# Kernel optimization log

Hardware: AMD Instinct MI355X
Metric: run time of the kernel (lower is better)

The kernel has to match this reference:

```python
import jax, jax.numpy as jnp
import numpy as np


def setup_inputs() -> dict:
    key = jax.random.key(0)
    ks = jax.random.split(key, 4)
    B, S, D, H, E = 4, 2048, 1024, 4096, 4
    sd = 1.0 / np.sqrt(D)
    sh = 1.0 / np.sqrt(H)
    return {
        "x": jax.random.normal(ks[0], (B, S, D), jnp.float32),
        "Wr": jax.random.normal(ks[1], (D, E), jnp.float32) * sd,
        "W1": jax.random.normal(ks[2], (E, D, H), jnp.float32) * sd,
        "b1": jnp.zeros((E, H), jnp.float32),
        "W2": jax.random.normal(ks[3], (E, H, D), jnp.float32) * sh,
        "b2": jnp.zeros((E, D), jnp.float32),
        "top_k": 2,
    }


def reference(x, Wr, W1, b1, W2, b2, top_k):
    # Router: softmax over experts, then top-k + renormalize (as in torch code)
    logits = jnp.einsum("bsd,de->bse", x, Wr)              # [B,S,E]
    probs = jax.nn.softmax(logits, axis=-1)
    wk, idx = jax.lax.top_k(probs, top_k)                  # [B,S,K]
    wk = wk / jnp.sum(wk, axis=-1, keepdims=True)
    # Scatter top-k weights back to dense per-expert weights [B,S,E]
    E = probs.shape[-1]
    onehot = jax.nn.one_hot(idx, E, dtype=x.dtype)         # [B,S,K,E]
    weights = jnp.einsum("bsk,bske->bse", wk, onehot)      # [B,S,E]
    # Expert MLPs (Linear-ReLU-Linear), computed dense over experts and
    # combined with the (mostly-zero) routing weights — same math as the
    # gather/scatter loop in the torch module.
    h = jax.nn.relu(jnp.einsum("bsd,edh->bseh", x, W1) + b1)   # [B,S,E,H]
    y = jnp.einsum("bseh,ehd->bsed", h, W2) + b2               # [B,S,E,D]
    out = jnp.einsum("bse,bsed->bsd", weights, y)              # [B,S,D]
    aux_loss = jnp.asarray(0.0, dtype=x.dtype)
    return out, aux_loss
```

## Files before the change

kernel.cpp:

```cpp
#include <hip/hip_runtime.h>
#include <cstdint>
#include <cstddef>

typedef _Float16 f16;
typedef __attribute__((ext_vector_type(8))) f16 f16x8;
typedef __attribute__((ext_vector_type(4))) f16 f16x4;
typedef __attribute__((ext_vector_type(4))) float f32x4;

#define M_TOK 8192
#define DDIM 1024
#define HDIM 4096
#define NEXP 4
#define TOTPAD 16896

__device__ __forceinline__ void async_copy16(const void* g, void* s) {
    __builtin_amdgcn_global_load_lds((__attribute__((address_space(1))) void*)g,
                                     (__attribute__((address_space(3))) void*)s,
                                     16, 0, 0);
}

__global__ __launch_bounds__(256) void router_kernel(
    const float* __restrict__ x, const float* __restrict__ Wr,
    float* __restrict__ wts, int* __restrict__ top2, float2* __restrict__ wpair) {
    __shared__ float wr_s[DDIM * NEXP];
    for (int i = threadIdx.x; i < DDIM * NEXP; i += 256) wr_s[i] = Wr[i];
    __syncthreads();
    const int wave = threadIdx.x >> 6, lane = threadIdx.x & 63;
    const int t = blockIdx.x * 4 + wave;
    float a0 = 0.f, a1 = 0.f, a2 = 0.f, a3 = 0.f;
    const float* xr = x + (size_t)t * DDIM;
    for (int i = 0; i < DDIM; i += 256) {
        const int d = i + lane * 4;
        const float4 v = *(const float4*)(xr + d);
        const float* w0 = &wr_s[d * 4];
        a0 += v.x * w0[0] + v.y * w0[4] + v.z * w0[8]  + v.w * w0[12];
        a1 += v.x * w0[1] + v.y * w0[5] + v.z * w0[9]  + v.w * w0[13];
        a2 += v.x * w0[2] + v.y * w0[6] + v.z * w0[10] + v.w * w0[14];
        a3 += v.x * w0[3] + v.y * w0[7] + v.z * w0[11] + v.w * w0[15];
    }
    for (int off = 32; off > 0; off >>= 1) {
        a0 += __shfl_xor(a0, off, 64);
        a1 += __shfl_xor(a1, off, 64);
        a2 += __shfl_xor(a2, off, 64);
        a3 += __shfl_xor(a3, off, 64);
    }
    if (lane == 0) {
        float lg[4] = {a0, a1, a2, a3};
        int i1 = 0;
        for (int e = 1; e < 4; ++e) if (lg[e] > lg[i1]) i1 = e;
        int i2 = -1;
        for (int e = 0; e < 4; ++e) {
            if (e == i1) continue;
            if (i2 < 0 || lg[e] > lg[i2]) i2 = e;
        }
        const float w1 = 1.0f / (1.0f + expf(lg[i2] - lg[i1]));
        float w[4] = {0.f, 0.f, 0.f, 0.f};
        w[i1] = w1; w[i2] = 1.0f - w1;
        float* o = wts + (size_t)t * 4;
        o[0] = w[0]; o[1] = w[1]; o[2] = w[2]; o[3] = w[3];
        top2[t] = i1 | (i2 << 8);
        wpair[t] = make_float2(w1, 1.0f - w1);
    }
}

__global__ __launch_bounds__(256) void count_kernel(
    const int* __restrict__ top2, int* __restrict__ meta) {
    __shared__ int lc[4];
    if (threadIdx.x < 4) lc[threadIdx.x] = 0;
    __syncthreads();
    const int t = blockIdx.x * 256 + threadIdx.x;
    const int p = top2[t];
    atomicAdd(&lc[p & 0xff], 1);
    atomicAdd(&lc[(p >> 8) & 0xff], 1);
    __syncthreads();
    if (threadIdx.x < 4) atomicAdd(&meta[threadIdx.x], lc[threadIdx.x]);
}

__global__ void offsets_kernel(int* __restrict__ meta) {
    if (threadIdx.x == 0) {
        int off = 0;
        for (int e = 0; e < 4; ++e) {
            const int c = meta[e];
            const int cp = (c + 127) & ~127;
            meta[4 + e] = cp;
            meta[8 + e] = off;
            off += cp;
        }
    }
}

__global__ __launch_bounds__(256) void fill_kernel(
    const int* __restrict__ top2, int* __restrict__ meta,
    int* __restrict__ toklist, int2* __restrict__ slotmap) {
    __shared__ int lc[4], base[4];
    if (threadIdx.x < 4) lc[threadIdx.x] = 0;
    __syncthreads();
    const int t = blockIdx.x * 256 + threadIdx.x;
    const int p = top2[t];
    const int e1 = p & 0xff, e2 = (p >> 8) & 0xff;
    const int r1 = atomicAdd(&lc[e1], 1);
    const int r2 = atomicAdd(&lc[e2], 1);
    __syncthreads();
    if (threadIdx.x < 4) base[threadIdx.x] = atomicAdd(&meta[12 + threadIdx.x], lc[threadIdx.x]);
    __syncthreads();
    const int p1 = meta[8 + e1] + base[e1] + r1;
    const int p2 = meta[8 + e2] + base[e2] + r2;
    toklist[p1] = t;
    toklist[p2] = t;
    slotmap[t] = make_int2(p1, p2);
}

__global__ __launch_bounds__(256) void convert_f16_kernel(
    const float* __restrict__ in, f16* __restrict__ out, int n4) {
    const int i = blockIdx.x * 256 + threadIdx.x;
    if (i < n4) {
        const float4 v = ((const float4*)in)[i];
        f16x4 o = {(f16)v.x, (f16)v.y, (f16)v.z, (f16)v.w};
        ((f16x4*)out)[i] = o;
    }
}

__global__ __launch_bounds__(256) void pack_b_kernel(
    const float* __restrict__ in0, f16* __restrict__ out0, int K, int N) {
    __shared__ float tile[64][65];
    const float* in = in0 + (size_t)blockIdx.z * K * N;
    f16* out = out0 + (size_t)blockIdx.z * K * N;
    const int n0 = blockIdx.x * 64, k0 = blockIdx.y * 64;
    const int tx = threadIdx.x & 63, ty = threadIdx.x >> 6;
#pragma unroll
    for (int i = 0; i < 64; i += 4)
        tile[ty + i][tx] = in[(size_t)(k0 + ty + i) * N + n0 + tx];
    __syncthreads();
#pragma unroll
    for (int c = 0; c < 2; ++c) {
        const int cc = c * 256 + threadIdx.x;
        const int grp = cc >> 7;
        const int within = cc & 127;
        const int kk2 = within >> 6, quad = (within >> 4) & 3, l16 = within & 15;
        const int nl = grp * 16 + l16;
        const int kl = kk2 * 32 + quad * 8;
        f16x8 v;
#pragma unroll
        for (int j = 0; j < 8; ++j) v[j] = (f16)tile[kl + j][nl];
        const size_t o = ((size_t)(n0 / 16 + grp) * (K >> 6) + (k0 >> 6)) * 1024 +
                         (size_t)within * 8;
        *(f16x8*)&out[o] = v;
    }
}

template <int MODE>
__global__ __launch_bounds__(256, 3) void gemm_kernel(
    const f16* __restrict__ A, const f16* __restrict__ Bswz,
    int N, int K,
    const float* __restrict__ bias,
    f16* __restrict__ outH, float* __restrict__ outF,
    const float* __restrict__ wts,
    const int* __restrict__ toklist, const int* __restrict__ meta, int e0) {
    __shared__ __align__(16) f16 As[2][128 * 64];
    const int zz = blockIdx.z;
    const int e = e0 + zz;
    const int m0 = blockIdx.x * 128, n0 = blockIdx.y * 128;

    int cnt = M_TOK, off = 0;
    if (meta) {
        cnt = meta[e];
        const int cp = meta[4 + e];
        off = meta[8 + e];
        if (m0 >= cp) return;
    }

    const f16* Be = Bswz + (size_t)zz * N * K;
    const float* be = bias + (size_t)zz * N;

    const int tid = threadIdx.x;
    const int wave = tid >> 6, lane = tid & 63;
    const int wm = wave >> 1, wn = wave & 1;
    const int quad = lane >> 4, l16 = lane & 15;
    const int Kb = K >> 6;

    f32x4 acc[4][4] = {};

    const int lrb = tid >> 3;
    const int gcoff = (((tid & 7) ^ (lrb & 7)) * 8);
    const f16* ga[4];
#pragma unroll
    for (int r = 0; r < 4; ++r) {
        const int gm = m0 + r * 32 + lrb;
        int arow;
        if (MODE == 0) arow = toklist ? toklist[off + gm] : gm;
        else arow = off + gm;
        ga[r] = A + (size_t)arow * K + gcoff;
    }

    const f16* bp[4];
#pragma unroll
    for (int j = 0; j < 4; ++j)
        bp[j] = Be + ((size_t)(n0 / 16 + wn * 4 + j) * Kb) * 1024 + lane * 8;

#pragma unroll
    for (int r = 0; r < 4; ++r)
        async_copy16(ga[r], &As[0][(r * 256 + tid) * 8]);
    __syncthreads();

    const int swl = l16 & 7;
    int p = 0;
    for (int k0b = 0; k0b < Kb; ++k0b) {
        f16x8 bf[2][4];
#pragma unroll
        for (int kk2 = 0; kk2 < 2; ++kk2)
#pragma unroll
            for (int j = 0; j < 4; ++j)
                bf[kk2][j] = *(const f16x8*)(bp[j] + (k0b << 10) + (kk2 << 9));

        if (k0b + 1 < Kb) {
            const int kn = (k0b + 1) << 6;
#pragma unroll
            for (int r = 0; r < 4; ++r)
                async_copy16(ga[r] + kn, &As[p ^ 1][(r * 256 + tid) * 8]);
        }

#pragma unroll
        for (int kk2 = 0; kk2 < 2; ++kk2) {
            f16x8 af[4];
#pragma unroll
            for (int i = 0; i < 4; ++i)
                af[i] = *(const f16x8*)&As[p][(size_t)(wm * 64 + i * 16 + l16) * 64 +
                                             (((kk2 * 4 + quad) ^ swl) << 3)];
#pragma unroll
            for (int i = 0; i < 4; ++i)
#pragma unroll
                for (int j = 0; j < 4; ++j)
                    acc[i][j] = __builtin_amdgcn_mfma_f32_16x16x32_f16(af[i], bf[kk2][j], acc[i][j], 0, 0, 0);
        }
        __syncthreads();
        p ^= 1;
    }

#pragma unroll
    for (int i = 0; i < 4; ++i) {
        const int mbase = m0 + wm * 64 + i * 16 + quad * 4;
#pragma unroll
        for (int j = 0; j < 4; ++j) {
            const int n = n0 + wn * 64 + j * 16 + l16;
            const float bv = be[n];
#pragma unroll
            for (int r = 0; r < 4; ++r) {
                const int m = mbase + r;
                float v = acc[i][j][r] + bv;
                if (MODE == 0) {
                    v = v > 0.0f ? v : 0.0f;
                    outH[(size_t)(off + m) * N + n] = (f16)v;
                } else {
                    if (outH) {
                        outH[(size_t)(off + m) * N + n] = (f16)v;
                    } else if (m < cnt) {
                        const float w = wts[m * 4 + e];
                        atomicAdd(&outF[(size_t)m * N + n], w * v);
                    }
                }
            }
        }
    }
}

__global__ __launch_bounds__(256) void combine_kernel(
    const f16* __restrict__ yseg, const int2* __restrict__ slotmap,
    const float2* __restrict__ wpair, float* __restrict__ out, int aux_idx) {
    const int t = blockIdx.x;
    const int2 p = slotmap[t];
    const float2 w = wpair[t];
    const int d = threadIdx.x * 4;
    const f16x4 a = *(const f16x4*)&yseg[(size_t)p.x * DDIM + d];
    const f16x4 b = *(const f16x4*)&yseg[(size_t)p.y * DDIM + d];
    float4 o;
    o.x = w.x * (float)a[0] + w.y * (float)b[0];
    o.y = w.x * (float)a[1] + w.y * (float)b[1];
    o.z = w.x * (float)a[2] + w.y * (float)b[2];
    o.w = w.x * (float)a[3] + w.y * (float)b[3];
    *(float4*)&out[(size_t)t * DDIM + d] = o;
    if (t == 0 && threadIdx.x == 0 && aux_idx >= 0) out[aux_idx] = 0.0f;
}

extern "C" void kernel_launch(void* const* d_in, const int* in_sizes, int n_in,
                              void* d_out, int out_size, void* d_ws, size_t ws_size,
                              hipStream_t stream) {
    (void)in_sizes; (void)n_in;
    const float* x  = (const float*)d_in[0];
    const float* Wr = (const float*)d_in[1];
    const float* W1 = (const float*)d_in[2];
    const float* b1 = (const float*)d_in[3];
    const float* W2 = (const float*)d_in[4];
    const float* b2 = (const float*)d_in[5];
    float* out = (float*)d_out;

    char* ws = (char*)d_ws;
    float*  wts   = (float*)ws;
    int*    meta  = (int*)(ws + (128 << 10));
    int*    top2  = (int*)(ws + (132 << 10));
    int*    tokl  = (int*)(ws + (164 << 10));
    float2* wpair = (float2*)(ws + (240 << 10));
    int2*   slotm = (int2*)(ws + (304 << 10));
    f16*    xb    = (f16*)(ws + (512 << 10));
    const size_t MBs = 1ull << 20;
    const size_t base = (512 << 10) + 16 * MBs;

    const size_t SPARSE_NEED = (512 << 10) + 80 * MBs + (size_t)TOTPAD * HDIM * sizeof(f16);
    const bool sparse = ws_size >= SPARSE_NEED;

    const int aux_idx = (out_size == M_TOK * DDIM + 1) ? (M_TOK * DDIM) : -1;

    f16 *w1t, *w2t, *h, *yseg;
    if (sparse) {
        w1t  = (f16*)(ws + base);
        w2t  = (f16*)(ws + base + 32 * MBs);
        h    = (f16*)(ws + base + 64 * MBs);
        yseg = (f16*)(ws + (512 << 10));
    } else {
        w1t = (f16*)(ws + base);
        w2t = (f16*)(ws + base + 8 * MBs);
        h   = (f16*)(ws + base + 16 * MBs);
        yseg = nullptr;
    }

    router_kernel<<<M_TOK / 4, 256, 0, stream>>>(x, Wr, wts, top2, wpair);
    convert_f16_kernel<<<(M_TOK * DDIM / 4) / 256, 256, 0, stream>>>(x, xb, M_TOK * DDIM / 4);

    if (sparse) {
        hipMemsetAsync(meta, 0, 16 * sizeof(int), stream);
        hipMemsetAsync(tokl, 0, (size_t)TOTPAD * sizeof(int), stream);
        count_kernel<<<M_TOK / 256, 256, 0, stream>>>(top2, meta);
        offsets_kernel<<<1, 64, 0, stream>>>(meta);
        fill_kernel<<<M_TOK / 256, 256, 0, stream>>>(top2, meta, tokl, slotm);
        pack_b_kernel<<<dim3(HDIM / 64, DDIM / 64, NEXP), 256, 0, stream>>>(W1, w1t, DDIM, HDIM);
        pack_b_kernel<<<dim3(DDIM / 64, HDIM / 64, NEXP), 256, 0, stream>>>(W2, w2t, HDIM, DDIM);
        gemm_kernel<0><<<dim3(M_TOK / 128, HDIM / 128, NEXP), 256, 0, stream>>>(
            xb, w1t, HDIM, DDIM, b1, h, nullptr, wts, tokl, meta, 0);
        gemm_kernel<1><<<dim3(M_TOK / 128, DDIM / 128, NEXP), 256, 0, stream>>>(
            h, w2t, DDIM, HDIM, b2, yseg, nullptr, wts, tokl, meta, 0);
        combine_kernel<<<M_TOK, 256, 0, stream>>>(yseg, slotm, wpair, out, aux_idx);
    } else {
        hipMemsetAsync(out, 0, (size_t)out_size * sizeof(float), stream);
        for (int e = 0; e < NEXP; ++e) {
            pack_b_kernel<<<dim3(HDIM / 64, DDIM / 64, 1), 256, 0, stream>>>(
                W1 + (size_t)e * DDIM * HDIM, w1t, DDIM, HDIM);
            gemm_kernel<0><<<dim3(M_TOK / 128, HDIM / 128, 1), 256, 0, stream>>>(
                xb, w1t, HDIM, DDIM, b1 + (size_t)e * HDIM, h, nullptr, wts, nullptr, nullptr, e);
            pack_b_kernel<<<dim3(DDIM / 64, HDIM / 64, 1), 256, 0, stream>>>(
                W2 + (size_t)e * HDIM * DDIM, w2t, HDIM, DDIM);
            gemm_kernel<1><<<dim3(M_TOK / 128, DDIM / 128, 1), 256, 0, stream>>>(
                h, w2t, DDIM, HDIM, b2 + (size_t)e * DDIM, nullptr, out, wts, nullptr, nullptr, e);
        }
    }
}
```

Baseline: 684.0 us.

## Replace 128x128 GEMM with 256x256 LDS-staged, ping-pong scheduled MFMA kernel

Swaps the expert GEMM for a 512-thread kernel with 256x256 output tiles. Both A and B are staged in LDS via async global-to-LDS copies in 32-wide K halves, and barriers plus setprio interleave the copies with MFMA bursts. The weight packing becomes a plain N-major transposed layout with XOR swizzle in LDS, and expert segments are padded to 256 rows. The larger tiles aim to raise arithmetic intensity and cut reloads of B, at the cost of more padding waste, more LDS and register use, and fewer blocks per CU.

```diff
diff --git a/kernel.cpp b/kernel.cpp
--- a/kernel.cpp
+++ b/kernel.cpp
@@ -11,12 +11,18 @@
 #define DDIM 1024
 #define HDIM 4096
 #define NEXP 4
-#define TOTPAD 16896
+#define TOTPAD 17408
 
 __device__ __forceinline__ void async_copy16(const void* g, void* s) {
     __builtin_amdgcn_global_load_lds((__attribute__((address_space(1))) void*)g,
                                      (__attribute__((address_space(3))) void*)s,
                                      16, 0, 0);
+}
+
+__device__ __forceinline__ void stage2(const f16* g0, const f16* g1, int koff,
+                                       f16* plane, int tid) {
+    async_copy16(g0 + koff, plane + tid * 8);
+    async_copy16(g1 + koff, plane + 4096 + tid * 8);
 }
 
 __global__ __launch_bounds__(256) void router_kernel(
@@ -81,7 +87,7 @@
         int off = 0;
         for (int e = 0; e < 4; ++e) {
             const int c = meta[e];
-            const int cp = (c + 127) & ~127;
+            const int cp = (c + 255) & ~255;
             meta[4 + e] = cp;
             meta[8 + e] = off;
             off += cp;
@@ -120,7 +126,7 @@
     }
 }
 
-__global__ __launch_bounds__(256) void pack_b_kernel(
+__global__ __launch_bounds__(256) void pack_nk_kernel(
     const float* __restrict__ in0, f16* __restrict__ out0, int K, int N) {
     __shared__ float tile[64][65];
     const float* in = in0 + (size_t)blockIdx.z * K * N;
@@ -134,118 +140,152 @@
 #pragma unroll
     for (int c = 0; c < 2; ++c) {
         const int cc = c * 256 + threadIdx.x;
-        const int grp = cc >> 7;
-        const int within = cc & 127;
-        const int kk2 = within >> 6, quad = (within >> 4) & 3, l16 = within & 15;
-        const int nl = grp * 16 + l16;
-        const int kl = kk2 * 32 + quad * 8;
+        const int nl = cc >> 3, kc = cc & 7;
         f16x8 v;
 #pragma unroll
-        for (int j = 0; j < 8; ++j) v[j] = (f16)tile[kl + j][nl];
-        const size_t o = ((size_t)(n0 / 16 + grp) * (K >> 6) + (k0 >> 6)) * 1024 +
-                         (size_t)within * 8;
-        *(f16x8*)&out[o] = v;
+        for (int j = 0; j < 8; ++j) v[j] = (f16)tile[kc * 8 + j][nl];
+        *(f16x8*)&out[(size_t)(n0 + nl) * K + k0 + kc * 8] = v;
     }
 }
 
 template <int MODE>
-__global__ __launch_bounds__(256, 3) void gemm_kernel(
-    const f16* __restrict__ A, const f16* __restrict__ Bswz,
-    int N, int K,
-    const float* __restrict__ bias,
-    f16* __restrict__ outH, float* __restrict__ outF,
-    const float* __restrict__ wts,
-    const int* __restrict__ toklist, const int* __restrict__ meta, int e0) {
-    __shared__ __align__(16) f16 As[2][128 * 64];
+__global__ __launch_bounds__(512, 2) void gemm256_kernel(
+    const f16* __restrict__ A, const f16* __restrict__ Bt, int N, int K,
+    const float* __restrict__ bias, f16* __restrict__ outH, float* __restrict__ outF,
+    const float* __restrict__ wts, const int* __restrict__ toklist,
+    const int* __restrict__ meta, int e0) {
+    __shared__ __align__(16) f16 S[2][32768];
     const int zz = blockIdx.z;
     const int e = e0 + zz;
-    const int m0 = blockIdx.x * 128, n0 = blockIdx.y * 128;
-
-    int cnt = M_TOK, off = 0;
-    if (meta) {
-        cnt = meta[e];
-        const int cp = meta[4 + e];
-        off = meta[8 + e];
-        if (m0 >= cp) return;
-    }
-
-    const f16* Be = Bswz + (size_t)zz * N * K;
+    const int m0 = blockIdx.x * 256, n0 = blockIdx.y * 256;
+    int cnt = M_TOK, cp = M_TOK, off = 0;
+    if (meta) { cnt = meta[e]; cp = meta[4 + e]; off = meta[8 + e]; }
+    if (m0 >= cp) return;
+
+    const f16* Be = Bt + (size_t)zz * N * K;
     const float* be = bias + (size_t)zz * N;
 
     const int tid = threadIdx.x;
     const int wave = tid >> 6, lane = tid & 63;
-    const int wm = wave >> 1, wn = wave & 1;
+    const int wm = wave >> 2, wn = wave & 3;
     const int quad = lane >> 4, l16 = lane & 15;
-    const int Kb = K >> 6;
-
-    f32x4 acc[4][4] = {};
-
-    const int lrb = tid >> 3;
-    const int gcoff = (((tid & 7) ^ (lrb & 7)) * 8);
-    const f16* ga[4];
-#pragma unroll
-    for (int r = 0; r < 4; ++r) {
-        const int gm = m0 + r * 32 + lrb;
+    const int NT = K >> 6;
+
+    const int r0 = tid >> 2;
+    const int gswz = ((tid & 3) ^ ((r0 >> 1) & 3)) * 8;
+    const f16* ga[2]; const f16* gb[2];
+#pragma unroll
+    for (int q = 0; q < 2; ++q) {
+        const int gm = m0 + q * 128 + r0;
         int arow;
         if (MODE == 0) arow = toklist ? toklist[off + gm] : gm;
         else arow = off + gm;
-        ga[r] = A + (size_t)arow * K + gcoff;
-    }
-
-    const f16* bp[4];
-#pragma unroll
-    for (int j = 0; j < 4; ++j)
-        bp[j] = Be + ((size_t)(n0 / 16 + wn * 4 + j) * Kb) * 1024 + lane * 8;
-
-#pragma unroll
-    for (int r = 0; r < 4; ++r)
-        async_copy16(ga[r], &As[0][(r * 256 + tid) * 8]);
-    __syncthreads();
-
-    const int swl = l16 & 7;
+        ga[q] = A + (size_t)arow * K + gswz;
+        gb[q] = Be + (size_t)(n0 + q * 128 + r0) * K + gswz;
+    }
+
+    const int chq = ((quad ^ ((l16 >> 1) & 3)) << 3);
+    const int a_base = (wm * 128 + l16) * 32 + chq;
+    const int b_base = 16384 + (wn * 64 + l16) * 32 + chq;
+
+    f32x4 acc[8][4] = {};
+
+    stage2(ga[0], ga[1], 0,  S[0] + 0,     tid);
+    stage2(gb[0], gb[1], 0,  S[0] + 16384, tid);
+    stage2(ga[0], ga[1], 32, S[0] + 8192,  tid);
+    stage2(gb[0], gb[1], 32, S[0] + 24576, tid);
+    if (NT > 1) {
+        stage2(ga[0], ga[1], 64, S[1] + 0,     tid);
+        stage2(gb[0], gb[1], 64, S[1] + 16384, tid);
+        stage2(ga[0], ga[1], 96, S[1] + 8192,  tid);
+        asm volatile("s_waitcnt vmcnt(6)" ::: "memory");
+    } else {
+        asm volatile("s_waitcnt vmcnt(0)" ::: "memory");
+    }
+    __builtin_amdgcn_s_barrier();
+
     int p = 0;
-    for (int k0b = 0; k0b < Kb; ++k0b) {
-        f16x8 bf[2][4];
-#pragma unroll
-        for (int kk2 = 0; kk2 < 2; ++kk2)
-#pragma unroll
-            for (int j = 0; j < 4; ++j)
-                bf[kk2][j] = *(const f16x8*)(bp[j] + (k0b << 10) + (kk2 << 9));
-
-        if (k0b + 1 < Kb) {
-            const int kn = (k0b + 1) << 6;
-#pragma unroll
-            for (int r = 0; r < 4; ++r)
-                async_copy16(ga[r] + kn, &As[p ^ 1][(r * 256 + tid) * 8]);
-        }
-
-#pragma unroll
-        for (int kk2 = 0; kk2 < 2; ++kk2) {
-            f16x8 af[4];
-#pragma unroll
-            for (int i = 0; i < 4; ++i)
-                af[i] = *(const f16x8*)&As[p][(size_t)(wm * 64 + i * 16 + l16) * 64 +
-                                             (((kk2 * 4 + quad) ^ swl) << 3)];
-#pragma unroll
-            for (int i = 0; i < 4; ++i)
-#pragma unroll
-                for (int j = 0; j < 4; ++j)
-                    acc[i][j] = __builtin_amdgcn_mfma_f32_16x16x32_f16(af[i], bf[kk2][j], acc[i][j], 0, 0, 0);
-        }
-        __syncthreads();
+#pragma unroll 1
+    for (int t = 0; t < NT; ++t) {
+        const f16* Sp = S[p];
+        f16* SpW = S[p];
+        f16* SoW = S[p ^ 1];
+        f16x8 af[8], bf0, bf1;
+#pragma unroll
+        for (int i = 0; i < 8; ++i) af[i] = *(const f16x8*)&Sp[a_base + i * 512];
+        bf0 = *(const f16x8*)&Sp[b_base];
+        bf1 = *(const f16x8*)&Sp[b_base + 512];
+        if (t + 1 < NT) stage2(gb[0], gb[1], ((t + 1) << 6) + 32, SoW + 24576, tid);
+        __builtin_amdgcn_s_barrier();
+        asm volatile("s_waitcnt lgkmcnt(0)" ::: "memory");
+        __builtin_amdgcn_sched_barrier(0);
+        __builtin_amdgcn_s_setprio(1);
+#pragma unroll
+        for (int i = 0; i < 8; ++i) {
+            acc[i][0] = __builtin_amdgcn_mfma_f32_16x16x32_f16(af[i], bf0, acc[i][0], 0, 0, 0);
+            acc[i][1] = __builtin_amdgcn_mfma_f32_16x16x32_f16(af[i], bf1, acc[i][1], 0, 0, 0);
+        }
+        __builtin_amdgcn_s_setprio(0);
+        __builtin_amdgcn_s_barrier();
+        bf0 = *(const f16x8*)&Sp[b_base + 1024];
+        bf1 = *(const f16x8*)&Sp[b_base + 1536];
+        if (t + 2 < NT) stage2(ga[0], ga[1], (t + 2) << 6, SpW, tid);
+        __builtin_amdgcn_s_barrier();
+        asm volatile("s_waitcnt lgkmcnt(0)" ::: "memory");
+        __builtin_amdgcn_sched_barrier(0);
+        __builtin_amdgcn_s_setprio(1);
+#pragma unroll
+        for (int i = 0; i < 8; ++i) {
+            acc[i][2] = __builtin_amdgcn_mfma_f32_16x16x32_f16(af[i], bf0, acc[i][2], 0, 0, 0);
+            acc[i][3] = __builtin_amdgcn_mfma_f32_16x16x32_f16(af[i], bf1, acc[i][3], 0, 0, 0);
+        }
+        __builtin_amdgcn_s_setprio(0);
+        __builtin_amdgcn_s_barrier();
+#pragma unroll
+        for (int i = 0; i < 8; ++i) af[i] = *(const f16x8*)&Sp[a_base + 8192 + i * 512];
+        bf0 = *(const f16x8*)&Sp[b_base + 8192];
+        bf1 = *(const f16x8*)&Sp[b_base + 8192 + 512];
+        if (t + 2 < NT) stage2(gb[0], gb[1], (t + 2) << 6, SpW + 16384, tid);
+        __builtin_amdgcn_s_barrier();
+        asm volatile("s_waitcnt lgkmcnt(0)" ::: "memory");
+        __builtin_amdgcn_sched_barrier(0);
+        __builtin_amdgcn_s_setprio(1);
+#pragma unroll
+        for (int i = 0; i < 8; ++i) {
+            acc[i][0] = __builtin_amdgcn_mfma_f32_16x16x32_f16(af[i], bf0, acc[i][0], 0, 0, 0);
+            acc[i][1] = __builtin_amdgcn_mfma_f32_16x16x32_f16(af[i], bf1, acc[i][1], 0, 0, 0);
+        }
+        __builtin_amdgcn_s_setprio(0);
+        __builtin_amdgcn_s_barrier();
+        bf0 = *(const f16x8*)&Sp[b_base + 8192 + 1024];
+        bf1 = *(const f16x8*)&Sp[b_base + 8192 + 1536];
+        if (t + 2 < NT) stage2(ga[0], ga[1], ((t + 2) << 6) + 32, SpW + 8192, tid);
+        __builtin_amdgcn_s_barrier();
+        asm volatile("s_waitcnt lgkmcnt(0)" ::: "memory");
+        __builtin_amdgcn_sched_barrier(0);
+        __builtin_amdgcn_s_setprio(1);
+#pragma unroll
+        for (int i = 0; i < 8; ++i) {
+            acc[i][2] = __builtin_amdgcn_mfma_f32_16x16x32_f16(af[i], bf0, acc[i][2], 0, 0, 0);
+            acc[i][3] = __builtin_amdgcn_mfma_f32_16x16x32_f16(af[i], bf1, acc[i][3], 0, 0, 0);
+        }
+        __builtin_amdgcn_s_setprio(0);
+        if (t + 2 < NT) asm volatile("s_waitcnt vmcnt(6)" ::: "memory");
+        else            asm volatile("s_waitcnt vmcnt(0)" ::: "memory");
+        __builtin_amdgcn_s_barrier();
         p ^= 1;
     }
 
 #pragma unroll
-    for (int i = 0; i < 4; ++i) {
-        const int mbase = m0 + wm * 64 + i * 16 + quad * 4;
+    for (int i = 0; i < 8; ++i) {
+        const int mb = m0 + wm * 128 + i * 16 + quad * 4;
 #pragma unroll
         for (int j = 0; j < 4; ++j) {
             const int n = n0 + wn * 64 + j * 16 + l16;
             const float bv = be[n];
 #pragma unroll
             for (int r = 0; r < 4; ++r) {
-                const int m = mbase + r;
+                const int m = mb + r;
                 float v = acc[i][j][r] + bv;
                 if (MODE == 0) {
                     v = v > 0.0f ? v : 0.0f;
@@ -254,8 +294,7 @@
                     if (outH) {
                         outH[(size_t)(off + m) * N + n] = (f16)v;
                     } else if (m < cnt) {
-                        const float w = wts[m * 4 + e];
-                        atomicAdd(&outF[(size_t)m * N + n], w * v);
+                        atomicAdd(&outF[(size_t)m * N + n], wts[m * 4 + e] * v);
                     }
                 }
             }
@@ -331,23 +370,24 @@
         count_kernel<<<M_TOK / 256, 256, 0, stream>>>(top2, meta);
         offsets_kernel<<<1, 64, 0, stream>>>(meta);
         fill_kernel<<<M_TOK / 256, 256, 0, stream>>>(top2, meta, tokl, slotm);
-        pack_b_kernel<<<dim3(HDIM / 64, DDIM / 64, NEXP), 256, 0, stream>>>(W1, w1t, DDIM, HDIM);
-        pack_b_kernel<<<dim3(DDIM / 64, HDIM / 64, NEXP), 256, 0, stream>>>(W2, w2t, HDIM, DDIM);
-        gemm_kernel<0><<<dim3(M_TOK / 128, HDIM / 128, NEXP), 256, 0, stream>>>(
+        pack_nk_kernel<<<dim3(HDIM / 64, DDIM / 64, NEXP), 256, 0, stream>>>(W1, w1t, DDIM, HDIM);
+        pack_nk_kernel<<<dim3(DDIM / 64, HDIM / 64, NEXP), 256, 0, stream>>>(W2, w2t, HDIM, DDIM);
+        const int GX = TOTPAD / 256;
+        gemm256_kernel<0><<<dim3(GX, HDIM / 256, NEXP), 512, 0, stream>>>(
             xb, w1t, HDIM, DDIM, b1, h, nullptr, wts, tokl, meta, 0);
-        gemm_kernel<1><<<dim3(M_TOK / 128, DDIM / 128, NEXP), 256, 0, stream>>>(
-            h, w2t, DDIM, HDIM, b2, yseg, nullptr, wts, tokl, meta, 0);
+        gemm256_kernel<1><<<dim3(GX, DDIM / 256, NEXP), 512, 0, stream>>>(
+            h, w2t, DDIM, HDIM, b2, yseg, nullptr, wts, nullptr, meta, 0);
         combine_kernel<<<M_TOK, 256, 0, stream>>>(yseg, slotm, wpair, out, aux_idx);
     } else {
         hipMemsetAsync(out, 0, (size_t)out_size * sizeof(float), stream);
         for (int e = 0; e < NEXP; ++e) {
-            pack_b_kernel<<<dim3(HDIM / 64, DDIM / 64, 1), 256, 0, stream>>>(
+            pack_nk_kernel<<<dim3(HDIM / 64, DDIM / 64, 1), 256, 0, stream>>>(
                 W1 + (size_t)e * DDIM * HDIM, w1t, DDIM, HDIM);
-            gemm_kernel<0><<<dim3(M_TOK / 128, HDIM / 128, 1), 256, 0, stream>>>(
+            gemm256_kernel<0><<<dim3(M_TOK / 256, HDIM / 256, 1), 512, 0, stream>>>(
                 xb, w1t, HDIM, DDIM, b1 + (size_t)e * HDIM, h, nullptr, wts, nullptr, nullptr, e);
-            pack_b_kernel<<<dim3(DDIM / 64, HDIM / 64, 1), 256, 0, stream>>>(
+            pack_nk_kernel<<<dim3(DDIM / 64, HDIM / 64, 1), 256, 0, stream>>>(
                 W2 + (size_t)e * HDIM * DDIM, w2t, HDIM, DDIM);
-            gemm_kernel<1><<<dim3(M_TOK / 128, DDIM / 128, 1), 256, 0, stream>>>(
+            gemm256_kernel<1><<<dim3(M_TOK / 256, DDIM / 256, 1), 512, 0, stream>>>(
                 h, w2t, DDIM, HDIM, b2 + (size_t)e * DDIM, nullptr, out, wts, nullptr, nullptr, e);
         }
     }
```

Result: faster. 643.3 us (-5.9%).
